# Performance work log

Measured on AMD Instinct MI355X. Metric: run time of the kernel, lower is better.

The kernel has to match this reference:

```python
import jax, jax.numpy as jnp
import numpy as np

ROPE_BASE = 10000.0
NEG_INF = -1e30


def _rope(x, positions):
    """x: [B, heads, D]; positions: [B] int. Matches PrecomputedRotaryEmbedding
    with emb = cat(freqs, freqs) and rotate-half."""
    D = x.shape[-1]
    half = D // 2
    inv_freq = 1.0 / (ROPE_BASE ** (jnp.arange(0, D, 2, dtype=jnp.float32) / D))  # [D/2]
    freqs = positions.astype(jnp.float32)[:, None] * inv_freq[None, :]            # [B, D/2]
    emb = jnp.concatenate([freqs, freqs], axis=-1)                                # [B, D]
    cos = jnp.cos(emb)[:, None, :]
    sin = jnp.sin(emb)[:, None, :]
    x1, x2 = x[..., :half], x[..., half:]
    rotated = jnp.concatenate([-x2, x1], axis=-1)
    return x * cos + rotated * sin


def setup_inputs() -> dict:
    key = jax.random.key(0)
    ks = jax.random.split(key, 6)
    B, H, Hkv, D = 32, 32, 8, 128
    block_size, max_blocks = 16, 256
    num_blocks = B * max_blocks  # 8192, disjoint blocks per sequence
    return {
        "query": jax.random.normal(ks[0], (B, H, D), dtype=jnp.float32),
        "key": jax.random.normal(ks[1], (B, Hkv, D), dtype=jnp.float32),
        "value": jax.random.normal(ks[2], (B, Hkv, D), dtype=jnp.float32),
        "k_cache": jax.random.normal(ks[3], (num_blocks, block_size, Hkv, D), dtype=jnp.float32),
        "v_cache": jax.random.normal(ks[4], (num_blocks, block_size, Hkv, D), dtype=jnp.float32),
        "block_table": jnp.arange(B * max_blocks, dtype=jnp.int32).reshape(B, max_blocks),
        "context_lens": jax.random.randint(ks[5], (B,), 1, 4096, dtype=jnp.int32),
        "block_size": block_size,
    }


def reference(query, key, value, k_cache, v_cache, block_table, context_lens, block_size):
    B, H, D = query.shape
    Hkv = key.shape[1]
    G = H // Hkv
    num_blocks, bs = k_cache.shape[0], k_cache.shape[1]
    scale = D ** -0.5

    # 1) RoPE at position = context_len (as in the original forward)
    q = _rope(query, context_lens)                      # [B, H, D]
    k_new = _rope(key, context_lens)                    # [B, Hkv, D]

    # 2) scatter-store new KV at slot of token (context_len - 1)
    last = context_lens - 1
    slots = block_table[jnp.arange(B), last // block_size] * block_size + last % block_size
    kc = k_cache.reshape(num_blocks * bs, Hkv, D).at[slots].set(k_new)
    vc = v_cache.reshape(num_blocks * bs, Hkv, D).at[slots].set(value)
    kc = kc.reshape(num_blocks, bs, Hkv, D)
    vc = vc.reshape(num_blocks, bs, Hkv, D)

    # 3) gather paged KV per sequence via block_table
    S = block_table.shape[1] * bs                       # max seq len
    Kg = kc[block_table].reshape(B, S, Hkv, D)          # [B, S, Hkv, D]
    Vg = vc[block_table].reshape(B, S, Hkv, D)

    # 4) GQA attention over valid positions [0, context_len)
    qg = q.reshape(B, Hkv, G, D)
    scores = jnp.einsum('bkgd,bskd->bkgs', qg, Kg) * scale   # [B, Hkv, G, S]
    valid = (jnp.arange(S)[None, :] < context_lens[:, None])  # [B, S]
    scores = jnp.where(valid[:, None, None, :], scores, NEG_INF)
    probs = jax.nn.softmax(scores, axis=-1)
    out = jnp.einsum('bkgs,bskd->bkgd', probs, Vg).reshape(B, H, D)
    return out
```

## Files before the change

kernel.cpp:

```cpp
#include <hip/hip_runtime.h>
#include <math.h>

namespace {
constexpr int B   = 32;
constexpr int H   = 32;
constexpr int HKV = 8;
constexpr int D   = 128;
constexpr int G   = H / HKV;
constexpr int BS  = 16;
constexpr int MAXB = 256;
constexpr int S   = BS * MAXB;
constexpr float SCALE = 0.08838834764831845f;
}

struct F8 { float v[8]; };

__device__ __forceinline__ F8 load8(const float* __restrict__ p) {
    F8 r;
    const float4 a = *reinterpret_cast<const float4*>(p);
    const float4 b = *reinterpret_cast<const float4*>(p + 4);
    r.v[0]=a.x; r.v[1]=a.y; r.v[2]=a.z; r.v[3]=a.w;
    r.v[4]=b.x; r.v[5]=b.y; r.v[6]=b.z; r.v[7]=b.w;
    return r;
}

__global__ void rope_kernel(const float* __restrict__ query,
                            const float* __restrict__ key,
                            const int*   __restrict__ ctx,
                            float* __restrict__ q_out,
                            float* __restrict__ k_out)
{
    const int row = blockIdx.x;
    const int t   = threadIdx.x;
    const bool is_q = row < B * H;
    const float* src;
    float* dst;
    int b;
    if (is_q) { b = row / H;  src = query + (size_t)row * D; dst = q_out + (size_t)row * D; }
    else      { int r = row - B * H; b = r / HKV;
                src = key + (size_t)r * D;  dst = k_out + (size_t)r * D; }
    const float pos = (float)ctx[b];
    const float inv = powf(10000.0f, -(2.0f * t) / (float)D);
    const float f = pos * inv;
    const float c = cosf(f), s = sinf(f);
    const float x1 = src[t], x2 = src[t + 64];
    float o1 = x1 * c - x2 * s;
    float o2 = x2 * c + x1 * s;
    if (is_q) { o1 *= SCALE; o2 *= SCALE; }
    dst[t]      = o1;
    dst[t + 64] = o2;
}

__global__ __launch_bounds__(256, 4)
void attn_kernel(const float* __restrict__ qr,
                 const float* __restrict__ kr,
                 const float* __restrict__ vnew,
                 const float* __restrict__ kc,
                 const float* __restrict__ vc,
                 const int*   __restrict__ bt,
                 const int*   __restrict__ ctx,
                 float* __restrict__ pl,
                 float* __restrict__ pa,
                 int chunk, int nch)
{
    const int c  = blockIdx.x;
    const int kv = blockIdx.y;
    const int b  = blockIdx.z;
    const int len = ctx[b];
    const int start = c * chunk;
    if (start >= len) return;
    const int end  = min(start + chunk, len);

    const int tid  = threadIdx.x;
    const int lane = tid & 63;
    const int wave = tid >> 6;
    const int sg   = lane >> 4;
    const int t    = lane & 15;
    const int wsub = wave * 4 + sg;

    F8 q[G];
    {
        const float* qbase = qr + ((size_t)b * H + kv * G) * D + t * 8;
        #pragma unroll
        for (int g = 0; g < G; ++g) q[g] = load8(qbase + g * D);
    }

    float l[G];
    F8 acc[G];
    #pragma unroll
    for (int g = 0; g < G; ++g) {
        l[g] = 0.f;
        #pragma unroll
        for (int j = 0; j < 8; ++j) acc[g].v[j] = 0.f;
    }

    const int* btb = bt + b * MAXB;

    auto process = [&](const F8& k, const F8& v) {
        #pragma unroll
        for (int g = 0; g < G; ++g) {
            float s = 0.f;
            #pragma unroll
            for (int j = 0; j < 8; ++j) s += q[g].v[j] * k.v[j];
            s += __shfl_xor(s, 1);
            s += __shfl_xor(s, 2);
            s += __shfl_xor(s, 4);
            s += __shfl_xor(s, 8);
            const float pv = __expf(s);
            l[g] += pv;
            #pragma unroll
            for (int j = 0; j < 8; ++j) acc[g].v[j] += pv * v.v[j];
        }
    };

    const int lim = (end == len) ? end - 1 : end;

    int p = start + wsub;
    if (p < lim) {
        int blk = btb[p >> 4];
        size_t r = ((size_t)(blk * BS + (p & 15)) * HKV + kv) * D + t * 8;
        F8 k = load8(kc + r), v = load8(vc + r);
        int pn = p + 16;
        while (pn < lim) {
            const int blk2 = btb[pn >> 4];
            const size_t r2 = ((size_t)(blk2 * BS + (pn & 15)) * HKV + kv) * D + t * 8;
            F8 kn = load8(kc + r2), vn = load8(vc + r2);
            process(k, v);
            k = kn; v = vn;
            pn += 16;
        }
        process(k, v);
    }

    if (end == len) {
        const int last = len - 1;
        if (((last - start) & 15) == wsub) {
            const size_t off = ((size_t)b * HKV + kv) * D + t * 8;
            F8 k = load8(kr + off), v = load8(vnew + off);
            process(k, v);
        }
    }

    #pragma unroll
    for (int g = 0; g < G; ++g) {
        l[g] += __shfl_xor(l[g], 16);
        l[g] += __shfl_xor(l[g], 32);
        #pragma unroll
        for (int j = 0; j < 8; ++j) {
            acc[g].v[j] += __shfl_xor(acc[g].v[j], 16);
            acc[g].v[j] += __shfl_xor(acc[g].v[j], 32);
        }
    }

    __shared__ float sm_l[4][G];
    __shared__ float sm_acc[4][G][D];
    if (sg == 0) {
        #pragma unroll
        for (int g = 0; g < G; ++g) {
            if (t == 0) sm_l[wave][g] = l[g];
            #pragma unroll
            for (int j = 0; j < 8; ++j) sm_acc[wave][g][t * 8 + j] = acc[g].v[j];
        }
    }
    __syncthreads();

    for (int idx = tid; idx < G * D; idx += 256) {
        const int g = idx >> 7, d = idx & 127;
        const float A = sm_acc[0][g][d] + sm_acc[1][g][d] +
                        sm_acc[2][g][d] + sm_acc[3][g][d];
        const size_t pi = (((size_t)b * HKV + kv) * nch + c) * G + g;
        if (d == 0)
            pl[pi] = sm_l[0][g] + sm_l[1][g] + sm_l[2][g] + sm_l[3][g];
        pa[pi * D + d] = A;
    }
}

__global__ void combine_kernel(const float* __restrict__ pl,
                               const float* __restrict__ pa,
                               const int*   __restrict__ ctx,
                               float* __restrict__ out,
                               int chunk, int nch)
{
    const int bk = blockIdx.x;
    const int b  = bk / HKV;
    const int kv = bk % HKV;
    const int len = ctx[b];
    const int nc = min(nch, (len + chunk - 1) / chunk);
    const int g = threadIdx.x >> 7;
    const int d = threadIdx.x & 127;

    const size_t base = (((size_t)b * HKV + kv) * nch) * G + g;
    float L = 0.f, A = 0.f;
    for (int c = 0; c < nc; ++c) {
        const size_t pi = base + (size_t)c * G;
        L += pl[pi];
        A += pa[pi * D + d];
    }
    out[((size_t)b * H + kv * G + g) * D + d] = A / L;
}

extern "C" void kernel_launch(void* const* d_in, const int* in_sizes, int n_in,
                              void* d_out, int out_size, void* d_ws, size_t ws_size,
                              hipStream_t stream) {
    const float* query   = (const float*)d_in[0];
    const float* key     = (const float*)d_in[1];
    const float* value   = (const float*)d_in[2];
    const float* k_cache = (const float*)d_in[3];
    const float* v_cache = (const float*)d_in[4];
    const int*   bt      = (const int*)d_in[5];
    const int*   ctx     = (const int*)d_in[6];
    float* out = (float*)d_out;
    float* ws  = (float*)d_ws;

    float* qr = ws;
    float* kr = qr + (size_t)B * H * D;
    float* pbase = kr + (size_t)B * HKV * D;

    const size_t fixed_bytes = ((size_t)B * H * D + (size_t)B * HKV * D) * 4;
    const size_t per_chunk   = (size_t)B * HKV * G * (1 + D) * 4;
    int nch = 16;
    if (ws_size < fixed_bytes + (size_t)nch * per_chunk) {
        size_t avail = (ws_size > fixed_bytes) ? (ws_size - fixed_bytes) : per_chunk;
        nch = (int)(avail / per_chunk);
        if (nch < 1) nch = 1;
    }
    const int chunk = (S + nch - 1) / nch;

    float* pl = pbase;
    float* pa = pl + (size_t)B * HKV * nch * G;

    rope_kernel<<<B * (H + HKV), 64, 0, stream>>>(query, key, ctx, qr, kr);

    dim3 grid(nch, HKV, B);
    attn_kernel<<<grid, 256, 0, stream>>>(qr, kr, value, k_cache, v_cache,
                                          bt, ctx, pl, pa, chunk, nch);

    combine_kernel<<<B * HKV, 512, 0, stream>>>(pl, pa, ctx, out, chunk, nch);
}
```

Measured before the change: 153.6 us.

## Fuse RoPE into attention kernel and raise split-K chunk count

Removes the separate RoPE kernel. Each attention block now computes cos/sin for its lanes and rotates q and the new key in registers, pairing halves with a lane shuffle. This drops one launch and the round trip of rotated q/k through workspace. The number of context chunks also doubles from 16 to 32, giving more parallelism at the cost of more partial results for the combine kernel to reduce, plus redundant trig in every block.

Result: slower. 210.1 us (+36.8%).

```diff
diff --git a/kernel.cpp b/kernel.cpp
--- a/kernel.cpp
+++ b/kernel.cpp
@@ -11,6 +11,7 @@
 constexpr int MAXB = 256;
 constexpr int S   = BS * MAXB;
 constexpr float SCALE = 0.08838834764831845f;
+constexpr float L2_1E4_OVER_64 = 0.2076205059304601f;
 }
 
 struct F8 { float v[8]; };
@@ -24,37 +25,10 @@
     return r;
 }
 
-__global__ void rope_kernel(const float* __restrict__ query,
-                            const float* __restrict__ key,
-                            const int*   __restrict__ ctx,
-                            float* __restrict__ q_out,
-                            float* __restrict__ k_out)
-{
-    const int row = blockIdx.x;
-    const int t   = threadIdx.x;
-    const bool is_q = row < B * H;
-    const float* src;
-    float* dst;
-    int b;
-    if (is_q) { b = row / H;  src = query + (size_t)row * D; dst = q_out + (size_t)row * D; }
-    else      { int r = row - B * H; b = r / HKV;
-                src = key + (size_t)r * D;  dst = k_out + (size_t)r * D; }
-    const float pos = (float)ctx[b];
-    const float inv = powf(10000.0f, -(2.0f * t) / (float)D);
-    const float f = pos * inv;
-    const float c = cosf(f), s = sinf(f);
-    const float x1 = src[t], x2 = src[t + 64];
-    float o1 = x1 * c - x2 * s;
-    float o2 = x2 * c + x1 * s;
-    if (is_q) { o1 *= SCALE; o2 *= SCALE; }
-    dst[t]      = o1;
-    dst[t + 64] = o2;
-}
-
 __global__ __launch_bounds__(256, 4)
-void attn_kernel(const float* __restrict__ qr,
-                 const float* __restrict__ kr,
-                 const float* __restrict__ vnew,
+void attn_kernel(const float* __restrict__ query,
+                 const float* __restrict__ key,
+                 const float* __restrict__ value,
                  const float* __restrict__ kc,
                  const float* __restrict__ vc,
                  const int*   __restrict__ bt,
@@ -78,12 +52,44 @@
     const int t    = lane & 15;
     const int wsub = wave * 4 + sg;
 
+    float cosv[8], sinv[8];
+    {
+        const float pos = (float)len;
+        const int i0 = (t & 7) * 8;
+        #pragma unroll
+        for (int j = 0; j < 8; ++j) {
+            const float inv = exp2f(-(float)(i0 + j) * L2_1E4_OVER_64);
+            const float f = pos * inv;
+            sinv[j] = sinf(f);
+            cosv[j] = cosf(f);
+        }
+    }
+    const float sgn = (t < 8) ? -1.f : 1.f;
+
+    auto rope8 = [&](F8 x) -> F8 {
+        F8 o;
+        #pragma unroll
+        for (int j = 0; j < 8; ++j) {
+            const float xp = __shfl_xor(x.v[j], 8);
+            o.v[j] = x.v[j] * cosv[j] + sgn * xp * sinv[j];
+        }
+        return o;
+    };
+
     F8 q[G];
     {
-        const float* qbase = qr + ((size_t)b * H + kv * G) * D + t * 8;
-        #pragma unroll
-        for (int g = 0; g < G; ++g) q[g] = load8(qbase + g * D);
-    }
+        const float* qbase = query + ((size_t)b * H + kv * G) * D + t * 8;
+        #pragma unroll
+        for (int g = 0; g < G; ++g) {
+            q[g] = rope8(load8(qbase + g * D));
+            #pragma unroll
+            for (int j = 0; j < 8; ++j) q[g].v[j] *= SCALE;
+        }
+    }
+
+    const size_t noff = ((size_t)b * HKV + kv) * D + t * 8;
+    const F8 knew = rope8(load8(key + noff));
+    const F8 vnw  = load8(value + noff);
 
     float l[G];
     F8 acc[G];
@@ -117,8 +123,8 @@
 
     int p = start + wsub;
     if (p < lim) {
-        int blk = btb[p >> 4];
-        size_t r = ((size_t)(blk * BS + (p & 15)) * HKV + kv) * D + t * 8;
+        const int blk = btb[p >> 4];
+        const size_t r = ((size_t)(blk * BS + (p & 15)) * HKV + kv) * D + t * 8;
         F8 k = load8(kc + r), v = load8(vc + r);
         int pn = p + 16;
         while (pn < lim) {
@@ -134,11 +140,7 @@
 
     if (end == len) {
         const int last = len - 1;
-        if (((last - start) & 15) == wsub) {
-            const size_t off = ((size_t)b * HKV + kv) * D + t * 8;
-            F8 k = load8(kr + off), v = load8(vnew + off);
-            process(k, v);
-        }
+        if (((last - start) & 15) == wsub) process(knew, vnw);
     }
 
     #pragma unroll
@@ -212,27 +214,19 @@
     float* out = (float*)d_out;
     float* ws  = (float*)d_ws;
 
-    float* qr = ws;
-    float* kr = qr + (size_t)B * H * D;
-    float* pbase = kr + (size_t)B * HKV * D;
-
-    const size_t fixed_bytes = ((size_t)B * H * D + (size_t)B * HKV * D) * 4;
-    const size_t per_chunk   = (size_t)B * HKV * G * (1 + D) * 4;
-    int nch = 16;
-    if (ws_size < fixed_bytes + (size_t)nch * per_chunk) {
-        size_t avail = (ws_size > fixed_bytes) ? (ws_size - fixed_bytes) : per_chunk;
-        nch = (int)(avail / per_chunk);
-        if (nch < 1) nch = 1;
+    const size_t per_chunk = (size_t)B * HKV * G * (1 + D) * 4;
+    int nch = 32;
+    if (ws_size < (size_t)nch * per_chunk) {
+        int fit = (int)(ws_size / per_chunk);
+        nch = fit < 1 ? 1 : fit;
     }
     const int chunk = (S + nch - 1) / nch;
 
-    float* pl = pbase;
+    float* pl = ws;
     float* pa = pl + (size_t)B * HKV * nch * G;
 
-    rope_kernel<<<B * (H + HKV), 64, 0, stream>>>(query, key, ctx, qr, kr);
-
     dim3 grid(nch, HKV, B);
-    attn_kernel<<<grid, 256, 0, stream>>>(qr, kr, value, k_cache, v_cache,
+    attn_kernel<<<grid, 256, 0, stream>>>(query, key, value, k_cache, v_cache,
                                           bt, ctx, pl, pa, chunk, nch);
 
     combine_kernel<<<B * HKV, 512, 0, stream>>>(pl, pa, ctx, out, chunk, nch);
```

## Map all KV heads into one block per chunk with finer chunking

Applied to the files above, without the earlier changes.

Each attention block now covers all 8 KV heads for one sequence chunk, with each 16-lane subgroup owning one KV head and one of two token parities. Grid becomes (chunks, B) and chunk size drops to 32 tokens, giving many more chunks. The aim is to read contiguous KV rows across heads (better coalescing of the Hkv*D row) and to spread short contexts across more blocks. In exchange, the combine kernel has many more partials to sum and more workspace is needed, with a fallback that doubles chunk size when workspace is short.

Result: slower. 164.8 us (+7.3%).

```diff
diff --git a/kernel.cpp b/kernel.cpp
--- a/kernel.cpp
+++ b/kernel.cpp
@@ -64,8 +64,7 @@
                  int chunk, int nch)
 {
     const int c  = blockIdx.x;
-    const int kv = blockIdx.y;
-    const int b  = blockIdx.z;
+    const int b  = blockIdx.y;
     const int len = ctx[b];
     const int start = c * chunk;
     if (start >= len) return;
@@ -77,6 +76,8 @@
     const int sg   = lane >> 4;
     const int t    = lane & 15;
     const int wsub = wave * 4 + sg;
+    const int kv   = wsub & 7;
+    const int par  = wsub >> 3;
 
     F8 q[G];
     {
@@ -113,64 +114,57 @@
         }
     };
 
-    const int lim = (end == len) ? end - 1 : end;
-
-    int p = start + wsub;
+    const int lim = (end == len) ? len - 1 : end;
+
+    auto addr = [&](int p) -> size_t {
+        const int blk = btb[p >> 4];
+        return ((size_t)(blk * BS + (p & 15)) * HKV + kv) * D + t * 8;
+    };
+
+    int p = start + par;
     if (p < lim) {
-        int blk = btb[p >> 4];
-        size_t r = ((size_t)(blk * BS + (p & 15)) * HKV + kv) * D + t * 8;
+        size_t r = addr(p);
         F8 k = load8(kc + r), v = load8(vc + r);
-        int pn = p + 16;
+        int pn = p + 2;
         while (pn < lim) {
-            const int blk2 = btb[pn >> 4];
-            const size_t r2 = ((size_t)(blk2 * BS + (pn & 15)) * HKV + kv) * D + t * 8;
+            const size_t r2 = addr(pn);
             F8 kn = load8(kc + r2), vn = load8(vc + r2);
             process(k, v);
             k = kn; v = vn;
-            pn += 16;
+            pn += 2;
         }
         process(k, v);
     }
 
     if (end == len) {
         const int last = len - 1;
-        if (((last - start) & 15) == wsub) {
+        if (((last - start) & 1) == par) {
             const size_t off = ((size_t)b * HKV + kv) * D + t * 8;
             F8 k = load8(kr + off), v = load8(vnew + off);
             process(k, v);
         }
     }
 
+    __shared__ float sm_l[16][G];
+    __shared__ float sm_acc[16][G][D];
+    if (t == 0) {
+        #pragma unroll
+        for (int g = 0; g < G; ++g) sm_l[wsub][g] = l[g];
+    }
     #pragma unroll
     for (int g = 0; g < G; ++g) {
-        l[g] += __shfl_xor(l[g], 16);
-        l[g] += __shfl_xor(l[g], 32);
-        #pragma unroll
-        for (int j = 0; j < 8; ++j) {
-            acc[g].v[j] += __shfl_xor(acc[g].v[j], 16);
-            acc[g].v[j] += __shfl_xor(acc[g].v[j], 32);
-        }
-    }
-
-    __shared__ float sm_l[4][G];
-    __shared__ float sm_acc[4][G][D];
-    if (sg == 0) {
-        #pragma unroll
-        for (int g = 0; g < G; ++g) {
-            if (t == 0) sm_l[wave][g] = l[g];
-            #pragma unroll
-            for (int j = 0; j < 8; ++j) sm_acc[wave][g][t * 8 + j] = acc[g].v[j];
-        }
+        #pragma unroll
+        for (int j = 0; j < 8; ++j) sm_acc[wsub][g][t * 8 + j] = acc[g].v[j];
     }
     __syncthreads();
 
-    for (int idx = tid; idx < G * D; idx += 256) {
-        const int g = idx >> 7, d = idx & 127;
-        const float A = sm_acc[0][g][d] + sm_acc[1][g][d] +
-                        sm_acc[2][g][d] + sm_acc[3][g][d];
-        const size_t pi = (((size_t)b * HKV + kv) * nch + c) * G + g;
-        if (d == 0)
-            pl[pi] = sm_l[0][g] + sm_l[1][g] + sm_l[2][g] + sm_l[3][g];
+    for (int idx = tid; idx < HKV * G * D; idx += 256) {
+        const int kvx = idx >> 9;
+        const int g   = (idx >> 7) & 3;
+        const int d   = idx & 127;
+        const float A = sm_acc[kvx][g][d] + sm_acc[8 + kvx][g][d];
+        const size_t pi = (((size_t)b * HKV + kvx) * nch + c) * G + g;
+        if (d == 0) pl[pi] = sm_l[kvx][g] + sm_l[8 + kvx][g];
         pa[pi * D + d] = A;
     }
 }
@@ -215,23 +209,24 @@
     float* qr = ws;
     float* kr = qr + (size_t)B * H * D;
     float* pbase = kr + (size_t)B * HKV * D;
-
     const size_t fixed_bytes = ((size_t)B * H * D + (size_t)B * HKV * D) * 4;
-    const size_t per_chunk   = (size_t)B * HKV * G * (1 + D) * 4;
-    int nch = 16;
-    if (ws_size < fixed_bytes + (size_t)nch * per_chunk) {
-        size_t avail = (ws_size > fixed_bytes) ? (ws_size - fixed_bytes) : per_chunk;
-        nch = (int)(avail / per_chunk);
-        if (nch < 1) nch = 1;
-    }
-    const int chunk = (S + nch - 1) / nch;
+
+    int chunk = 32;
+    int nch = (S + chunk - 1) / chunk;
+    auto need = [&](int n) {
+        return fixed_bytes + (size_t)B * HKV * n * G * (1 + D) * 4;
+    };
+    while (need(nch) > ws_size && chunk < S) {
+        chunk *= 2;
+        nch = (S + chunk - 1) / chunk;
+    }
 
     float* pl = pbase;
     float* pa = pl + (size_t)B * HKV * nch * G;
 
     rope_kernel<<<B * (H + HKV), 64, 0, stream>>>(query, key, ctx, qr, kr);
 
-    dim3 grid(nch, HKV, B);
+    dim3 grid(nch, B);
     attn_kernel<<<grid, 256, 0, stream>>>(qr, kr, value, k_cache, v_cache,
                                           bt, ctx, pl, pa, chunk, nch);
 
```

## Split attention into 64-token chunks with fully unrolled KV loads

Applied to the files above, without the earlier changes.

The sequence is now split into 64-token chunks instead of 16 chunks of 256 tokens, which gives many more workgroups for the paged-attention pass. Each wave subgroup then covers exactly four positions. The four block-table entries and row addresses are computed up front, and the K/V loads are issued in an unrolled software-pipelined sequence instead of a dynamic while-loop, so more memory requests are in flight at once. In exchange, more partial results are written and the combine kernel has more chunks to reduce. The unrolled path also only covers 64 positions, so the fallback that doubles the chunk size when workspace is short would silently skip tokens.

New measurement: 151.6 us (median of 2 runs). Within noise of the previous version (-1.3%).

```diff
diff --git a/kernel.cpp b/kernel.cpp
--- a/kernel.cpp
+++ b/kernel.cpp
@@ -70,6 +70,7 @@
     const int start = c * chunk;
     if (start >= len) return;
     const int end  = min(start + chunk, len);
+    const int lim  = (end == len) ? len - 1 : end;
 
     const int tid  = threadIdx.x;
     const int lane = tid & 63;
@@ -94,7 +95,14 @@
         for (int j = 0; j < 8; ++j) acc[g].v[j] = 0.f;
     }
 
-    const int* btb = bt + b * MAXB;
+    const int* btb = bt + b * MAXB + (start >> 4);
+    const int e0 = btb[0], e1 = btb[1], e2 = btb[2], e3 = btb[3];
+
+    auto rowaddr = [&](int e) -> size_t {
+        return ((size_t)(e * BS + wsub) * HKV + kv) * D + t * 8;
+    };
+    const size_t a0 = rowaddr(e0), a1 = rowaddr(e1),
+                 a2 = rowaddr(e2), a3 = rowaddr(e3);
 
     auto process = [&](const F8& k, const F8& v) {
         #pragma unroll
@@ -113,32 +121,26 @@
         }
     };
 
-    const int lim = (end == len) ? end - 1 : end;
-
-    int p = start + wsub;
-    if (p < lim) {
-        int blk = btb[p >> 4];
-        size_t r = ((size_t)(blk * BS + (p & 15)) * HKV + kv) * D + t * 8;
-        F8 k = load8(kc + r), v = load8(vc + r);
-        int pn = p + 16;
-        while (pn < lim) {
-            const int blk2 = btb[pn >> 4];
-            const size_t r2 = ((size_t)(blk2 * BS + (pn & 15)) * HKV + kv) * D + t * 8;
-            F8 kn = load8(kc + r2), vn = load8(vc + r2);
-            process(k, v);
-            k = kn; v = vn;
-            pn += 16;
-        }
+    const int pw = start + wsub;
+    const bool v0 = pw      < lim;
+    const bool v1 = pw + 16 < lim;
+    const bool v2 = pw + 32 < lim;
+    const bool v3 = pw + 48 < lim;
+
+    F8 kk, vv;
+    if (v0) { kk = load8(kc + a0); vv = load8(vc + a0); }
+    if (v1) { F8 kn = load8(kc + a1), vn = load8(vc + a1);
+              process(kk, vv); kk = kn; vv = vn; }
+    if (v2) { F8 kn = load8(kc + a2), vn = load8(vc + a2);
+              process(kk, vv); kk = kn; vv = vn; }
+    if (v3) { F8 kn = load8(kc + a3), vn = load8(vc + a3);
+              process(kk, vv); kk = kn; vv = vn; }
+    if (v0) process(kk, vv);
+
+    if (end == len && ((len - 1 - start) & 15) == wsub) {
+        const size_t off = ((size_t)b * HKV + kv) * D + t * 8;
+        F8 k = load8(kr + off), v = load8(vnew + off);
         process(k, v);
-    }
-
-    if (end == len) {
-        const int last = len - 1;
-        if (((last - start) & 15) == wsub) {
-            const size_t off = ((size_t)b * HKV + kv) * D + t * 8;
-            F8 k = load8(kr + off), v = load8(vnew + off);
-            process(k, v);
-        }
     }
 
     #pragma unroll
@@ -215,16 +217,17 @@
     float* qr = ws;
     float* kr = qr + (size_t)B * H * D;
     float* pbase = kr + (size_t)B * HKV * D;
-
     const size_t fixed_bytes = ((size_t)B * H * D + (size_t)B * HKV * D) * 4;
-    const size_t per_chunk   = (size_t)B * HKV * G * (1 + D) * 4;
-    int nch = 16;
-    if (ws_size < fixed_bytes + (size_t)nch * per_chunk) {
-        size_t avail = (ws_size > fixed_bytes) ? (ws_size - fixed_bytes) : per_chunk;
-        nch = (int)(avail / per_chunk);
-        if (nch < 1) nch = 1;
-    }
-    const int chunk = (S + nch - 1) / nch;
+
+    int chunk = 64;
+    int nch = (S + chunk - 1) / chunk;
+    auto need = [&](int n) {
+        return fixed_bytes + (size_t)B * HKV * n * G * (1 + D) * 4;
+    };
+    while (need(nch) > ws_size && chunk < S) {
+        chunk *= 2;
+        nch = (S + chunk - 1) / chunk;
+    }
 
     float* pl = pbase;
     float* pa = pl + (size_t)B * HKV * nch * G;
```
